# Kernel optimization log

Hardware: AMD Instinct MI355X
Metric: run time of the kernel (lower is better)

## Reference

```python
import jax, jax.numpy as jnp
import numpy as np

D_MODEL = 1024
N_HEAD = 16
D_K = D_MODEL // N_HEAD
NEG = -1e9


def setup_inputs() -> dict:
    key = jax.random.key(0)
    ks = jax.random.split(key, 9)
    B, S = 2, 2048
    scale = 1.0 / np.sqrt(D_MODEL)
    x = jax.random.normal(ks[0], (B, S, D_MODEL), dtype=jnp.float32)
    mask = jnp.tril(jnp.ones((S, S), dtype=jnp.int32))  # causal: 0 => masked
    Wq = jax.random.normal(ks[1], (D_MODEL, D_MODEL), dtype=jnp.float32) * scale
    bq = jnp.zeros((D_MODEL,), dtype=jnp.float32)
    Wk = jax.random.normal(ks[2], (D_MODEL, D_MODEL), dtype=jnp.float32) * scale
    bk = jnp.zeros((D_MODEL,), dtype=jnp.float32)
    Wv = jax.random.normal(ks[3], (D_MODEL, D_MODEL), dtype=jnp.float32) * scale
    bv = jnp.zeros((D_MODEL,), dtype=jnp.float32)
    Wo = jax.random.normal(ks[4], (D_MODEL, D_MODEL), dtype=jnp.float32) * scale
    bo = jnp.zeros((D_MODEL,), dtype=jnp.float32)
    return {"x": x, "mask": mask, "Wq": Wq, "bq": bq, "Wk": Wk, "bk": bk,
            "Wv": Wv, "bv": bv, "Wo": Wo, "bo": bo}


def reference(x, mask, Wq, bq, Wk, bk, Wv, bv, Wo, bo):
    B, S, _ = x.shape
    # torch Linear: y = x @ W.T + b
    def split_heads(y):  # [B,S,D] -> [B,H,S,d_k]
        return y.reshape(B, S, N_HEAD, D_K).transpose(0, 2, 1, 3)
    Q = split_heads(x @ Wq.T + bq)
    K = split_heads(x @ Wk.T + bk)
    V = split_heads(x @ Wv.T + bv)
    scores = jnp.einsum('bhqd,bhkd->bhqk', Q, K) / jnp.sqrt(jnp.float32(D_K))
    scores = jnp.where(mask[None, None, :, :] == 0, jnp.float32(NEG), scores)
    attn = jax.nn.softmax(scores, axis=-1)
    out = jnp.einsum('bhqk,bhkd->bhqd', attn, V)
    out = out.transpose(0, 2, 1, 3).reshape(B, S, D_MODEL)
    return out @ Wo.T + bo
```

## Files before the change

kernel.cpp:

```cpp
#include <hip/hip_runtime.h>
#include <hip/hip_bf16.h>
#include <stdint.h>

#define DM    1024
#define NHEAD 16
#define DKH   64
#define SEQ   2048
#define NB    2
#define MTOT  (NB*SEQ)
#define LSTR  72
#define QSCL  0.18033688f

typedef __hip_bfloat16 bf16;
typedef __attribute__((ext_vector_type(8))) short bf16x8;
typedef __attribute__((ext_vector_type(4))) short bf16x4;
typedef __attribute__((ext_vector_type(4))) float f32x4;
typedef __attribute__((ext_vector_type(4))) uint32_t u32x4;

#define MFMA16(a,b,c) __builtin_amdgcn_mfma_f32_16x16x32_bf16((a),(b),(c),0,0,0)

#if __has_builtin(__builtin_amdgcn_exp2f)
#define EXP2F(x) __builtin_amdgcn_exp2f(x)
#else
#define EXP2F(x) __expf(0.69314718056f * (x))
#endif

__device__ __forceinline__ void async_copy16(const void* g, void* l) {
  __builtin_amdgcn_global_load_lds((const __attribute__((address_space(1))) uint32_t*)g,
                                   (__attribute__((address_space(3))) uint32_t*)l,
                                   16, 0, 0);
}

__device__ __forceinline__ short f32_bf16_bits(float f) {
  uint32_t u = __builtin_bit_cast(uint32_t, f);
  u += 0x7FFFu + ((u >> 16) & 1u);
  return (short)(u >> 16);
}

__device__ __forceinline__ uint32_t pack_bf16x2(float a, float b) {
  return (uint32_t)(uint16_t)f32_bf16_bits(a) |
         ((uint32_t)(uint16_t)f32_bf16_bits(b) << 16);
}

__global__ __launch_bounds__(256) void k_cvt_all(
    const float* __restrict__ x,  const float* __restrict__ Wq,
    const float* __restrict__ Wk, const float* __restrict__ Wv,
    const float* __restrict__ Wo,
    bf16* __restrict__ xb,  bf16* __restrict__ Wqb, bf16* __restrict__ Wkb,
    bf16* __restrict__ Wvb, bf16* __restrict__ Wob) {
  const int NX = (MTOT*DM)/4;
  const int NW = (DM*DM)/4;
  int i = blockIdx.x * 256 + threadIdx.x;
  const float* s; bf16* d; int j; float scl = 1.0f;
  if (i < NX) { s = x; d = xb; j = i; }
  else {
    int t = i - NX;
    int k = t >> 18;
    j = t & (NW - 1);
    s = (k == 0) ? Wq : (k == 1) ? Wk : (k == 2) ? Wv : Wo;
    d = (k == 0) ? Wqb : (k == 1) ? Wkb : (k == 2) ? Wvb : Wob;
    if (k == 0) scl = QSCL;
  }
  float4 v = ((const float4*)s)[j];
  bf16x4 o;
  o[0] = f32_bf16_bits(v.x * scl);
  o[1] = f32_bf16_bits(v.y * scl);
  o[2] = f32_bf16_bits(v.z * scl);
  o[3] = f32_bf16_bits(v.w * scl);
  ((bf16x4*)d)[j] = o;
}

__global__ __launch_bounds__(256) void k_gemm_qkv(
    const bf16* __restrict__ x,
    const bf16* __restrict__ Wq, const bf16* __restrict__ Wk, const bf16* __restrict__ Wv,
    const float* __restrict__ bq, const float* __restrict__ bk, const float* __restrict__ bv,
    bf16* __restrict__ Q, bf16* __restrict__ K, bf16* __restrict__ V) {
  const int id  = blockIdx.x + (blockIdx.y << 5) + (blockIdx.z << 8);
  const int xcd = id & 7;
  const int jj  = id >> 3;
  const int bxi = (xcd << 2) | (jj & 3);
  const int rem = jj >> 2;
  const int byi = rem & 7;
  const int bzi = rem >> 3;

  const bf16* W; const float* bias; bf16* C; float bs;
  if (bzi == 0)      { W = Wq; bias = bq; C = Q; bs = QSCL; }
  else if (bzi == 1) { W = Wk; bias = bk; C = K; bs = 1.0f; }
  else               { W = Wv; bias = bv; C = V; bs = 1.0f; }

  __shared__ __align__(16) short As[128*32];
  __shared__ __align__(16) short Bs[128*32];
  const int tid  = threadIdx.x;
  const int lane = tid & 63;
  const int w    = tid >> 6;
  const int wm   = (w & 1) << 6;
  const int wn   = (w >> 1) << 6;
  const int bm   = bxi << 7;
  const int bn   = byi << 7;
  const int m16  = lane & 15;
  const int quad = lane >> 4;
  const int koff = quad << 3;
  const int c0   = (w << 7) | lane;

  f32x4 acc[4][4] = {};

  for (int k0 = 0; k0 < DM; k0 += 32) {
    __syncthreads();
#pragma unroll
    for (int it = 0; it < 2; ++it) {
      int c   = c0 + (it << 6);
      int row = c >> 2;
      int kc  = c & 3;
      async_copy16(x + (size_t)(bm + row) * DM + k0 + (kc << 3),
                   &As[(size_t)((w << 7) + (it << 6)) << 3]);
      async_copy16(W + (size_t)(bn + row) * DM + k0 + (kc << 3),
                   &Bs[(size_t)((w << 7) + (it << 6)) << 3]);
    }
    __syncthreads();

    bf16x8 af[4], bfv[4];
#pragma unroll
    for (int t = 0; t < 4; ++t)
      af[t]  = *(const bf16x8*)&As[(wm + t*16 + m16) * 32 + koff];
#pragma unroll
    for (int t = 0; t < 4; ++t)
      bfv[t] = *(const bf16x8*)&Bs[(wn + t*16 + m16) * 32 + koff];
#pragma unroll
    for (int i = 0; i < 4; ++i)
#pragma unroll
      for (int j = 0; j < 4; ++j)
        acc[i][j] = MFMA16(af[i], bfv[j], acc[i][j]);
  }

  const int crow0 = bm + wm + (quad << 2);
  const int ccol0 = bn + wn + m16;
#pragma unroll
  for (int j = 0; j < 4; ++j) {
    float bv = bias[ccol0 + j*16] * bs;
#pragma unroll
    for (int i = 0; i < 4; ++i)
#pragma unroll
      for (int r = 0; r < 4; ++r)
        C[(size_t)(crow0 + i*16 + r) * DM + ccol0 + j*16] =
            (bf16)(acc[i][j][r] + bv);
  }
}

__global__ __launch_bounds__(256) void k_gemm_o(
    const bf16* __restrict__ A, const bf16* __restrict__ W,
    const float* __restrict__ bias, float* __restrict__ C) {
  const int id  = blockIdx.x + (blockIdx.y << 5);
  const int xcd = id & 7;
  const int jj  = id >> 3;
  const int bxi = (xcd << 2) | (jj & 3);
  const int byi = jj >> 2;

  __shared__ __align__(16) short As[128*32];
  __shared__ __align__(16) short Bs[64*32];
  const int tid  = threadIdx.x;
  const int lane = tid & 63;
  const int w    = tid >> 6;
  const int wm   = (w & 1) << 6;
  const int wn   = (w >> 1) << 5;
  const int bm   = bxi << 7;
  const int bn   = byi << 6;
  const int m16  = lane & 15;
  const int quad = lane >> 4;
  const int koff = quad << 3;
  const int cA   = (w << 7) | lane;
  const int cB   = (w << 6) | lane;

  f32x4 acc[4][2] = {};

  for (int k0 = 0; k0 < DM; k0 += 32) {
    __syncthreads();
#pragma unroll
    for (int it = 0; it < 2; ++it) {
      int c   = cA + (it << 6);
      int row = c >> 2;
      int kc  = c & 3;
      async_copy16(A + (size_t)(bm + row) * DM + k0 + (kc << 3),
                   &As[(size_t)((w << 7) + (it << 6)) << 3]);
    }
    {
      int row = cB >> 2;
      int kc  = cB & 3;
      async_copy16(W + (size_t)(bn + row) * DM + k0 + (kc << 3),
                   &Bs[(size_t)(w << 6) << 3]);
    }
    __syncthreads();

    bf16x8 af[4], bfv[2];
#pragma unroll
    for (int t = 0; t < 4; ++t)
      af[t]  = *(const bf16x8*)&As[(wm + t*16 + m16) * 32 + koff];
#pragma unroll
    for (int t = 0; t < 2; ++t)
      bfv[t] = *(const bf16x8*)&Bs[(wn + t*16 + m16) * 32 + koff];
#pragma unroll
    for (int i = 0; i < 4; ++i)
#pragma unroll
      for (int j = 0; j < 2; ++j)
        acc[i][j] = MFMA16(af[i], bfv[j], acc[i][j]);
  }

  const int crow0 = bm + wm + (quad << 2);
  const int ccol0 = bn + wn + m16;
#pragma unroll
  for (int j = 0; j < 2; ++j) {
    float bv = bias[ccol0 + j*16];
#pragma unroll
    for (int i = 0; i < 4; ++i)
#pragma unroll
      for (int r = 0; r < 4; ++r)
        C[(size_t)(crow0 + i*16 + r) * DM + ccol0 + j*16] =
            acc[i][j][r] + bv;
  }
}

__global__ __launch_bounds__(256) void k_transpose_v(const bf16* __restrict__ V,
                                                     bf16* __restrict__ Vt) {
  __shared__ __align__(16) short tile[64][LSTR];
  const int tid = threadIdx.x;
  const int s0  = blockIdx.x << 6;
  const int bh  = blockIdx.y;
  const int b   = bh >> 4, h = bh & 15;
#pragma unroll
  for (int it = 0; it < 2; ++it) {
    int c = tid + (it << 8);
    int s = c >> 3, dc = c & 7;
    bf16x8 v = *(const bf16x8*)&V[(size_t)(b*SEQ + s0 + s) * DM + h*DKH + (dc << 3)];
    *(bf16x8*)&tile[s][dc << 3] = v;
  }
  __syncthreads();
#pragma unroll
  for (int it = 0; it < 2; ++it) {
    int c = tid + (it << 8);
    int d = c >> 3, sc = c & 7;
    bf16x8 ov;
#pragma unroll
    for (int i = 0; i < 8; ++i) {
      int p  = (sc << 3) + i;
      int r  = p & 3;
      int st = ((p >> 5) & 1) | (((p >> 2) & 1) << 1);
      int q2 = (p >> 3) & 3;
      ov[i] = tile[st*16 + q2*4 + r][d];
    }
    *(bf16x8*)&Vt[((size_t)bh * DKH + d) * SEQ + s0 + (sc << 3)] = ov;
  }
}

__global__ __launch_bounds__(256) void k_attn(const bf16* __restrict__ Q,
                                              const bf16* __restrict__ K,
                                              const bf16* __restrict__ Vt,
                                              bf16* __restrict__ ctx) {
  __shared__ __align__(16) short Ks[64*LSTR];
  __shared__ __align__(16) short Vs[64*LSTR];

  const int tid  = threadIdx.x;
  const int lane = tid & 63;
  const int w    = tid >> 6;
  const int bh   = blockIdx.y;
  const int mx   = (blockIdx.x ^ bh) & 31;
  const int t64  = (mx & 1) ? (31 - (mx >> 1)) : (mx >> 1);
  const int b    = bh >> 4, h = bh & 15;
  const int m16  = lane & 15, quad = lane >> 4;
  const int koff = quad << 3;

  const int qw    = (t64 << 6) + (w << 4);
  const int ktmax = t64;

  const int r0 = tid >> 3, r1 = r0 + 32, c0 = (tid & 7) << 3;

  const bf16* Kb  = K  + (size_t)(b*SEQ) * DM + h*DKH;
  const bf16* Vtb = Vt + (size_t)bh * DKH * SEQ;

  const bf16* Qb = Q + (size_t)(b*SEQ + qw) * DM + h*DKH;
  bf16x8 qf0 = *(const bf16x8*)(Qb + (size_t)m16*DM + koff);
  bf16x8 qf1 = *(const bf16x8*)(Qb + (size_t)m16*DM + 32 + koff);

  f32x4 o[4] = {};
  float psum = 0.f;
  const int qrow  = qw + m16;
  const int kquad = quad << 2;

  bf16x8 pk0 = *(const bf16x8*)(Kb  + (size_t)r0*DM + c0);
  bf16x8 pk1 = *(const bf16x8*)(Kb  + (size_t)r1*DM + c0);
  bf16x8 pv0 = *(const bf16x8*)(Vtb + (size_t)r0*SEQ + c0);
  bf16x8 pv1 = *(const bf16x8*)(Vtb + (size_t)r1*SEQ + c0);

  for (int kt = 0; kt <= ktmax; ++kt) {
    __syncthreads();
    *(bf16x8*)&Ks[r0*LSTR + c0] = pk0;
    *(bf16x8*)&Ks[r1*LSTR + c0] = pk1;
    *(bf16x8*)&Vs[r0*LSTR + c0] = pv0;
    *(bf16x8*)&Vs[r1*LSTR + c0] = pv1;
    __syncthreads();

    if (kt < ktmax) {
      const int kn = (kt + 1) << 6;
      pk0 = *(const bf16x8*)(Kb  + (size_t)(kn + r0)*DM + c0);
      pk1 = *(const bf16x8*)(Kb  + (size_t)(kn + r1)*DM + c0);
      pv0 = *(const bf16x8*)(Vtb + (size_t)r0*SEQ + kn + c0);
      pv1 = *(const bf16x8*)(Vtb + (size_t)r1*SEQ + kn + c0);
    }

    {
      u32x4 p0, p1;
      const int kbase = (kt << 6) + kquad;
      if (kt == ktmax) {
#pragma unroll
        for (int st = 0; st < 4; ++st) {
          bf16x8 kf0 = *(const bf16x8*)&Ks[(st*16 + m16)*LSTR + koff];
          bf16x8 kf1 = *(const bf16x8*)&Ks[(st*16 + m16)*LSTR + 32 + koff];
          f32x4 a = {};
          a = MFMA16(kf0, qf0, a);
          a = MFMA16(kf1, qf1, a);
          float e[4];
#pragma unroll
          for (int r = 0; r < 4; ++r) {
            float t = EXP2F(a[r]);
            t = (kbase + (st << 4) + r <= qrow) ? t : 0.f;
            e[r] = t; psum += t;
          }
          uint32_t lo = pack_bf16x2(e[0], e[1]);
          uint32_t hi = pack_bf16x2(e[2], e[3]);
          int base = st & 2;
          if (st & 1) { p1[base] = lo; p1[base + 1] = hi; }
          else        { p0[base] = lo; p0[base + 1] = hi; }
        }
      } else {
#pragma unroll
        for (int st = 0; st < 4; ++st) {
          bf16x8 kf0 = *(const bf16x8*)&Ks[(st*16 + m16)*LSTR + koff];
          bf16x8 kf1 = *(const bf16x8*)&Ks[(st*16 + m16)*LSTR + 32 + koff];
          f32x4 a = {};
          a = MFMA16(kf0, qf0, a);
          a = MFMA16(kf1, qf1, a);
          float e[4];
#pragma unroll
          for (int r = 0; r < 4; ++r) {
            float t = EXP2F(a[r]);
            e[r] = t; psum += t;
          }
          uint32_t lo = pack_bf16x2(e[0], e[1]);
          uint32_t hi = pack_bf16x2(e[2], e[3]);
          int base = st & 2;
          if (st & 1) { p1[base] = lo; p1[base + 1] = hi; }
          else        { p0[base] = lo; p0[base + 1] = hi; }
        }
      }
      bf16x8 pa0 = __builtin_bit_cast(bf16x8, p0);
      bf16x8 pa1 = __builtin_bit_cast(bf16x8, p1);
#pragma unroll
      for (int t = 0; t < 4; ++t) {
        bf16x8 vf0 = *(const bf16x8*)&Vs[(t*16 + m16)*LSTR + koff];
        bf16x8 vf1 = *(const bf16x8*)&Vs[(t*16 + m16)*LSTR + 32 + koff];
        o[t] = MFMA16(pa0, vf0, o[t]);
        o[t] = MFMA16(pa1, vf1, o[t]);
      }
    }
  }

  float v = psum;
  v += __shfl_xor(v, 16, 64);
  v += __shfl_xor(v, 32, 64);
  const int lanebase = lane & 48;
  bf16* Cb = ctx + (size_t)(b*SEQ + qw) * DM + h*DKH;
#pragma unroll
  for (int r = 0; r < 4; ++r) {
    float rs  = __shfl(v, lanebase | (kquad | r), 64);
    float inv = 1.0f / rs;
#pragma unroll
    for (int t = 0; t < 4; ++t)
      Cb[(size_t)(kquad + r) * DM + t*16 + m16] = (bf16)(o[t][r] * inv);
  }
}

extern "C" void kernel_launch(void* const* d_in, const int* in_sizes, int n_in,
                              void* d_out, int out_size, void* d_ws, size_t ws_size,
                              hipStream_t stream) {
  const float* x  = (const float*)d_in[0];
  const float* Wq = (const float*)d_in[2];
  const float* bq = (const float*)d_in[3];
  const float* Wk = (const float*)d_in[4];
  const float* bk = (const float*)d_in[5];
  const float* Wv = (const float*)d_in[6];
  const float* bv = (const float*)d_in[7];
  const float* Wo = (const float*)d_in[8];
  const float* bo = (const float*)d_in[9];
  float* out = (float*)d_out;

  const size_t SZ = (size_t)MTOT * DM;
  const size_t WZ = (size_t)DM * DM;
  bf16* xb  = (bf16*)d_ws;
  bf16* Wqb = xb  + SZ;
  bf16* Wkb = Wqb + WZ;
  bf16* Wvb = Wkb + WZ;
  bf16* Wob = Wvb + WZ;
  bf16* Qb  = Wob + WZ;
  bf16* Kb  = Qb  + SZ;
  bf16* Vb  = Kb  + SZ;
  bf16* Vtb = Vb  + SZ;
  bf16* Cx  = xb;

  k_cvt_all<<<(SZ/4 + 4*(WZ/4))/256, 256, 0, stream>>>(
      x, Wq, Wk, Wv, Wo, xb, Wqb, Wkb, Wvb, Wob);

  k_gemm_qkv<<<dim3(MTOT/128, DM/128, 3), 256, 0, stream>>>(
      xb, Wqb, Wkb, Wvb, bq, bk, bv, Qb, Kb, Vb);
  k_transpose_v<<<dim3(SEQ/64, NB*NHEAD), 256, 0, stream>>>(Vb, Vtb);
  k_attn<<<dim3(32, NB*NHEAD), 256, 0, stream>>>(Qb, Kb, Vtb, Cx);
  k_gemm_o<<<dim3(MTOT/128, DM/64), 256, 0, stream>>>(Cx, Wob, bo, out);
}
```

Before: 201.8 us.

## Process two 16-row query tiles per wave in causal attention kernel

Each attention block now covers 128 query rows instead of 64, with each wave computing two 16-row Q tiles against every K/V tile staged in shared memory. This halves K/V loads and LDS reads per query row and raises MFMA work per synchronization. The grid halves to 16 blocks per head, and masking now applies to the last two key tiles. The trade-off is higher register pressure, fewer blocks for occupancy, and coarser causal load balancing.

```diff
diff --git a/kernel.cpp b/kernel.cpp
--- a/kernel.cpp
+++ b/kernel.cpp
@@ -261,14 +261,15 @@
   const int lane = tid & 63;
   const int w    = tid >> 6;
   const int bh   = blockIdx.y;
-  const int mx   = (blockIdx.x ^ bh) & 31;
-  const int t64  = (mx & 1) ? (31 - (mx >> 1)) : (mx >> 1);
+  const int mx   = (blockIdx.x ^ bh) & 15;
+  const int t64  = (mx & 1) ? (15 - (mx >> 1)) : (mx >> 1);
   const int b    = bh >> 4, h = bh & 15;
   const int m16  = lane & 15, quad = lane >> 4;
   const int koff = quad << 3;
 
-  const int qw    = (t64 << 6) + (w << 4);
-  const int ktmax = t64;
+  const int qw    = (t64 << 7) + (w << 5);
+  const int ktmax = 2*t64 + 1;
+  const int kdiag = 2*t64;
 
   const int r0 = tid >> 3, r1 = r0 + 32, c0 = (tid & 7) << 3;
 
@@ -276,12 +277,15 @@
   const bf16* Vtb = Vt + (size_t)bh * DKH * SEQ;
 
   const bf16* Qb = Q + (size_t)(b*SEQ + qw) * DM + h*DKH;
-  bf16x8 qf0 = *(const bf16x8*)(Qb + (size_t)m16*DM + koff);
-  bf16x8 qf1 = *(const bf16x8*)(Qb + (size_t)m16*DM + 32 + koff);
-
-  f32x4 o[4] = {};
-  float psum = 0.f;
-  const int qrow  = qw + m16;
+  bf16x8 qf0a = *(const bf16x8*)(Qb + (size_t)m16*DM + koff);
+  bf16x8 qf1a = *(const bf16x8*)(Qb + (size_t)m16*DM + 32 + koff);
+  bf16x8 qf0b = *(const bf16x8*)(Qb + (size_t)(16 + m16)*DM + koff);
+  bf16x8 qf1b = *(const bf16x8*)(Qb + (size_t)(16 + m16)*DM + 32 + koff);
+
+  f32x4 oa[4] = {}, ob[4] = {};
+  float psa = 0.f, psb = 0.f;
+  const int qrowa = qw + m16;
+  const int qrowb = qw + 16 + m16;
   const int kquad = quad << 2;
 
   bf16x8 pk0 = *(const bf16x8*)(Kb  + (size_t)r0*DM + c0);
@@ -306,74 +310,107 @@
     }
 
     {
-      u32x4 p0, p1;
+      u32x4 p0a, p1a, p0b, p1b;
       const int kbase = (kt << 6) + kquad;
-      if (kt == ktmax) {
+      if (kt >= kdiag) {
 #pragma unroll
         for (int st = 0; st < 4; ++st) {
           bf16x8 kf0 = *(const bf16x8*)&Ks[(st*16 + m16)*LSTR + koff];
           bf16x8 kf1 = *(const bf16x8*)&Ks[(st*16 + m16)*LSTR + 32 + koff];
-          f32x4 a = {};
-          a = MFMA16(kf0, qf0, a);
-          a = MFMA16(kf1, qf1, a);
-          float e[4];
+          f32x4 aa = {}, ab = {};
+          aa = MFMA16(kf0, qf0a, aa);
+          aa = MFMA16(kf1, qf1a, aa);
+          ab = MFMA16(kf0, qf0b, ab);
+          ab = MFMA16(kf1, qf1b, ab);
+          float ea[4], eb[4];
 #pragma unroll
           for (int r = 0; r < 4; ++r) {
-            float t = EXP2F(a[r]);
-            t = (kbase + (st << 4) + r <= qrow) ? t : 0.f;
-            e[r] = t; psum += t;
+            int key = kbase + (st << 4) + r;
+            float ta = EXP2F(aa[r]);
+            ta = (key <= qrowa) ? ta : 0.f;
+            ea[r] = ta; psa += ta;
+            float tb = EXP2F(ab[r]);
+            tb = (key <= qrowb) ? tb : 0.f;
+            eb[r] = tb; psb += tb;
           }
-          uint32_t lo = pack_bf16x2(e[0], e[1]);
-          uint32_t hi = pack_bf16x2(e[2], e[3]);
           int base = st & 2;
-          if (st & 1) { p1[base] = lo; p1[base + 1] = hi; }
-          else        { p0[base] = lo; p0[base + 1] = hi; }
+          uint32_t loa = pack_bf16x2(ea[0], ea[1]);
+          uint32_t hia = pack_bf16x2(ea[2], ea[3]);
+          uint32_t lob = pack_bf16x2(eb[0], eb[1]);
+          uint32_t hib = pack_bf16x2(eb[2], eb[3]);
+          if (st & 1) { p1a[base] = loa; p1a[base+1] = hia;
+                        p1b[base] = lob; p1b[base+1] = hib; }
+          else        { p0a[base] = loa; p0a[base+1] = hia;
+                        p0b[base] = lob; p0b[base+1] = hib; }
         }
       } else {
 #pragma unroll
         for (int st = 0; st < 4; ++st) {
           bf16x8 kf0 = *(const bf16x8*)&Ks[(st*16 + m16)*LSTR + koff];
           bf16x8 kf1 = *(const bf16x8*)&Ks[(st*16 + m16)*LSTR + 32 + koff];
-          f32x4 a = {};
-          a = MFMA16(kf0, qf0, a);
-          a = MFMA16(kf1, qf1, a);
-          float e[4];
+          f32x4 aa = {}, ab = {};
+          aa = MFMA16(kf0, qf0a, aa);
+          aa = MFMA16(kf1, qf1a, aa);
+          ab = MFMA16(kf0, qf0b, ab);
+          ab = MFMA16(kf1, qf1b, ab);
+          float ea[4], eb[4];
 #pragma unroll
           for (int r = 0; r < 4; ++r) {
-            float t = EXP2F(a[r]);
-            e[r] = t; psum += t;
+            float ta = EXP2F(aa[r]);
+            ea[r] = ta; psa += ta;
+            float tb = EXP2F(ab[r]);
+            eb[r] = tb; psb += tb;
           }
-          uint32_t lo = pack_bf16x2(e[0], e[1]);
-          uint32_t hi = pack_bf16x2(e[2], e[3]);
           int base = st & 2;
-          if (st & 1) { p1[base] = lo; p1[base + 1] = hi; }
-          else        { p0[base] = lo; p0[base + 1] = hi; }
+          uint32_t loa = pack_bf16x2(ea[0], ea[1]);
+          uint32_t hia = pack_bf16x2(ea[2], ea[3]);
+          uint32_t lob = pack_bf16x2(eb[0], eb[1]);
+          uint32_t hib = pack_bf16x2(eb[2], eb[3]);
+          if (st & 1) { p1a[base] = loa; p1a[base+1] = hia;
+                        p1b[base] = lob; p1b[base+1] = hib; }
+          else        { p0a[base] = loa; p0a[base+1] = hia;
+                        p0b[base] = lob; p0b[base+1] = hib; }
         }
       }
-      bf16x8 pa0 = __builtin_bit_cast(bf16x8, p0);
-      bf16x8 pa1 = __builtin_bit_cast(bf16x8, p1);
+      bf16x8 pa0a = __builtin_bit_cast(bf16x8, p0a);
+      bf16x8 pa1a = __builtin_bit_cast(bf16x8, p1a);
+      bf16x8 pa0b = __builtin_bit_cast(bf16x8, p0b);
+      bf16x8 pa1b = __builtin_bit_cast(bf16x8, p1b);
 #pragma unroll
       for (int t = 0; t < 4; ++t) {
         bf16x8 vf0 = *(const bf16x8*)&Vs[(t*16 + m16)*LSTR + koff];
         bf16x8 vf1 = *(const bf16x8*)&Vs[(t*16 + m16)*LSTR + 32 + koff];
-        o[t] = MFMA16(pa0, vf0, o[t]);
-        o[t] = MFMA16(pa1, vf1, o[t]);
+        oa[t] = MFMA16(pa0a, vf0, oa[t]);
+        oa[t] = MFMA16(pa1a, vf1, oa[t]);
+        ob[t] = MFMA16(pa0b, vf0, ob[t]);
+        ob[t] = MFMA16(pa1b, vf1, ob[t]);
       }
     }
   }
 
-  float v = psum;
-  v += __shfl_xor(v, 16, 64);
-  v += __shfl_xor(v, 32, 64);
+  float va = psa;
+  va += __shfl_xor(va, 16, 64);
+  va += __shfl_xor(va, 32, 64);
+  float vb = psb;
+  vb += __shfl_xor(vb, 16, 64);
+  vb += __shfl_xor(vb, 32, 64);
   const int lanebase = lane & 48;
   bf16* Cb = ctx + (size_t)(b*SEQ + qw) * DM + h*DKH;
 #pragma unroll
   for (int r = 0; r < 4; ++r) {
-    float rs  = __shfl(v, lanebase | (kquad | r), 64);
-    float inv = 1.0f / rs;
+    float rsa = __shfl(va, lanebase | (kquad | r), 64);
+    float inva = 1.0f / rsa;
 #pragma unroll
     for (int t = 0; t < 4; ++t)
-      Cb[(size_t)(kquad + r) * DM + t*16 + m16] = (bf16)(o[t][r] * inv);
+      Cb[(size_t)(kquad + r) * DM + t*16 + m16] = (bf16)(oa[t][r] * inva);
+  }
+#pragma unroll
+  for (int r = 0; r < 4; ++r) {
+    float rsb = __shfl(vb, lanebase | (kquad | r), 64);
+    float invb = 1.0f / rsb;
+#pragma unroll
+    for (int t = 0; t < 4; ++t)
+      Cb[(size_t)(16 + kquad + r) * DM + t*16 + m16] = (bf16)(ob[t][r] * invb);
   }
 }
 
@@ -410,6 +447,6 @@
   k_gemm_qkv<<<dim3(MTOT/128, DM/128, 3), 256, 0, stream>>>(
       xb, Wqb, Wkb, Wvb, bq, bk, bv, Qb, Kb, Vb);
   k_transpose_v<<<dim3(SEQ/64, NB*NHEAD), 256, 0, stream>>>(Vb, Vtb);
-  k_attn<<<dim3(32, NB*NHEAD), 256, 0, stream>>>(Qb, Kb, Vtb, Cx);
+  k_attn<<<dim3(16, NB*NHEAD), 256, 0, stream>>>(Qb, Kb, Vtb, Cx);
   k_gemm_o<<<dim3(MTOT/128, DM/64), 256, 0, stream>>>(Cx, Wob, bo, out);
 }
```

Measured after the change: 211.0 us. 4.5% more time.

## Process attention key tiles in pairs with doubled LDS staging

Applied to the files above, without the earlier changes.

The attention kernel now stages two 64-key K/V tiles into shared memory per iteration and prefetches the next two tiles into registers, which halves the number of barrier pairs and deepens the global-load prefetch. An odd trailing tile is handled in a separate epilogue with masking. The cost is doubled shared memory per block and more live prefetch registers, which may lower occupancy. Out-of-range prefetches are clamped to the last tile, so some loads are redundant.

```diff
diff --git a/kernel.cpp b/kernel.cpp
--- a/kernel.cpp
+++ b/kernel.cpp
@@ -254,8 +254,10 @@
                                               const bf16* __restrict__ K,
                                               const bf16* __restrict__ Vt,
                                               bf16* __restrict__ ctx) {
-  __shared__ __align__(16) short Ks[64*LSTR];
-  __shared__ __align__(16) short Vs[64*LSTR];
+  __shared__ __align__(16) short KsA[64*LSTR];
+  __shared__ __align__(16) short VsA[64*LSTR];
+  __shared__ __align__(16) short KsB[64*LSTR];
+  __shared__ __align__(16) short VsB[64*LSTR];
 
   const int tid  = threadIdx.x;
   const int lane = tid & 63;
@@ -284,82 +286,116 @@
   const int qrow  = qw + m16;
   const int kquad = quad << 2;
 
-  bf16x8 pk0 = *(const bf16x8*)(Kb  + (size_t)r0*DM + c0);
-  bf16x8 pk1 = *(const bf16x8*)(Kb  + (size_t)r1*DM + c0);
-  bf16x8 pv0 = *(const bf16x8*)(Vtb + (size_t)r0*SEQ + c0);
-  bf16x8 pv1 = *(const bf16x8*)(Vtb + (size_t)r1*SEQ + c0);
-
-  for (int kt = 0; kt <= ktmax; ++kt) {
-    __syncthreads();
-    *(bf16x8*)&Ks[r0*LSTR + c0] = pk0;
-    *(bf16x8*)&Ks[r1*LSTR + c0] = pk1;
-    *(bf16x8*)&Vs[r0*LSTR + c0] = pv0;
-    *(bf16x8*)&Vs[r1*LSTR + c0] = pv1;
-    __syncthreads();
-
-    if (kt < ktmax) {
-      const int kn = (kt + 1) << 6;
-      pk0 = *(const bf16x8*)(Kb  + (size_t)(kn + r0)*DM + c0);
-      pk1 = *(const bf16x8*)(Kb  + (size_t)(kn + r1)*DM + c0);
-      pv0 = *(const bf16x8*)(Vtb + (size_t)r0*SEQ + kn + c0);
-      pv1 = *(const bf16x8*)(Vtb + (size_t)r1*SEQ + kn + c0);
-    }
-
+  auto attn_tile = [&](const short* Kc, const short* Vc, int kt, bool masked) {
+    u32x4 p0, p1;
+    const int kbase = (kt << 6) + kquad;
+    if (masked) {
+#pragma unroll
+      for (int st = 0; st < 4; ++st) {
+        bf16x8 kf0 = *(const bf16x8*)&Kc[(st*16 + m16)*LSTR + koff];
+        bf16x8 kf1 = *(const bf16x8*)&Kc[(st*16 + m16)*LSTR + 32 + koff];
+        f32x4 a = {};
+        a = MFMA16(kf0, qf0, a);
+        a = MFMA16(kf1, qf1, a);
+        float e[4];
+#pragma unroll
+        for (int r = 0; r < 4; ++r) {
+          float t = EXP2F(a[r]);
+          t = (kbase + (st << 4) + r <= qrow) ? t : 0.f;
+          e[r] = t; psum += t;
+        }
+        uint32_t lo = pack_bf16x2(e[0], e[1]);
+        uint32_t hi = pack_bf16x2(e[2], e[3]);
+        int base = st & 2;
+        if (st & 1) { p1[base] = lo; p1[base + 1] = hi; }
+        else        { p0[base] = lo; p0[base + 1] = hi; }
+      }
+    } else {
+#pragma unroll
+      for (int st = 0; st < 4; ++st) {
+        bf16x8 kf0 = *(const bf16x8*)&Kc[(st*16 + m16)*LSTR + koff];
+        bf16x8 kf1 = *(const bf16x8*)&Kc[(st*16 + m16)*LSTR + 32 + koff];
+        f32x4 a = {};
+        a = MFMA16(kf0, qf0, a);
+        a = MFMA16(kf1, qf1, a);
+        float e[4];
+#pragma unroll
+        for (int r = 0; r < 4; ++r) {
+          float t = EXP2F(a[r]);
+          e[r] = t; psum += t;
+        }
+        uint32_t lo = pack_bf16x2(e[0], e[1]);
+        uint32_t hi = pack_bf16x2(e[2], e[3]);
+        int base = st & 2;
+        if (st & 1) { p1[base] = lo; p1[base + 1] = hi; }
+        else        { p0[base] = lo; p0[base + 1] = hi; }
+      }
+    }
+    bf16x8 pa0 = __builtin_bit_cast(bf16x8, p0);
+    bf16x8 pa1 = __builtin_bit_cast(bf16x8, p1);
+#pragma unroll
+    for (int t = 0; t < 4; ++t) {
+      bf16x8 vf0 = *(const bf16x8*)&Vc[(t*16 + m16)*LSTR + koff];
+      bf16x8 vf1 = *(const bf16x8*)&Vc[(t*16 + m16)*LSTR + 32 + koff];
+      o[t] = MFMA16(pa0, vf0, o[t]);
+      o[t] = MFMA16(pa1, vf1, o[t]);
+    }
+  };
+
+  bf16x8 kA0, kA1, vA0, vA1, kB0, kB1, vB0, vB1;
+  {
+    const int kn1 = (ktmax >= 1 ? 1 : 0) << 6;
+    kA0 = *(const bf16x8*)(Kb  + (size_t)r0*DM + c0);
+    kA1 = *(const bf16x8*)(Kb  + (size_t)r1*DM + c0);
+    vA0 = *(const bf16x8*)(Vtb + (size_t)r0*SEQ + c0);
+    vA1 = *(const bf16x8*)(Vtb + (size_t)r1*SEQ + c0);
+    kB0 = *(const bf16x8*)(Kb  + (size_t)(kn1 + r0)*DM + c0);
+    kB1 = *(const bf16x8*)(Kb  + (size_t)(kn1 + r1)*DM + c0);
+    vB0 = *(const bf16x8*)(Vtb + (size_t)r0*SEQ + kn1 + c0);
+    vB1 = *(const bf16x8*)(Vtb + (size_t)r1*SEQ + kn1 + c0);
+  }
+
+  const int ntiles = ktmax + 1;
+  const int npairs = ntiles >> 1;
+
+  for (int p = 0; p < npairs; ++p) {
+    __syncthreads();
+    *(bf16x8*)&KsA[r0*LSTR + c0] = kA0;
+    *(bf16x8*)&KsA[r1*LSTR + c0] = kA1;
+    *(bf16x8*)&VsA[r0*LSTR + c0] = vA0;
+    *(bf16x8*)&VsA[r1*LSTR + c0] = vA1;
+    *(bf16x8*)&KsB[r0*LSTR + c0] = kB0;
+    *(bf16x8*)&KsB[r1*LSTR + c0] = kB1;
+    *(bf16x8*)&VsB[r0*LSTR + c0] = vB0;
+    *(bf16x8*)&VsB[r1*LSTR + c0] = vB1;
+    __syncthreads();
+
+    const int ktA = 2*p, ktB = 2*p + 1;
     {
-      u32x4 p0, p1;
-      const int kbase = (kt << 6) + kquad;
-      if (kt == ktmax) {
-#pragma unroll
-        for (int st = 0; st < 4; ++st) {
-          bf16x8 kf0 = *(const bf16x8*)&Ks[(st*16 + m16)*LSTR + koff];
-          bf16x8 kf1 = *(const bf16x8*)&Ks[(st*16 + m16)*LSTR + 32 + koff];
-          f32x4 a = {};
-          a = MFMA16(kf0, qf0, a);
-          a = MFMA16(kf1, qf1, a);
-          float e[4];
-#pragma unroll
-          for (int r = 0; r < 4; ++r) {
-            float t = EXP2F(a[r]);
-            t = (kbase + (st << 4) + r <= qrow) ? t : 0.f;
-            e[r] = t; psum += t;
-          }
-          uint32_t lo = pack_bf16x2(e[0], e[1]);
-          uint32_t hi = pack_bf16x2(e[2], e[3]);
-          int base = st & 2;
-          if (st & 1) { p1[base] = lo; p1[base + 1] = hi; }
-          else        { p0[base] = lo; p0[base + 1] = hi; }
-        }
-      } else {
-#pragma unroll
-        for (int st = 0; st < 4; ++st) {
-          bf16x8 kf0 = *(const bf16x8*)&Ks[(st*16 + m16)*LSTR + koff];
-          bf16x8 kf1 = *(const bf16x8*)&Ks[(st*16 + m16)*LSTR + 32 + koff];
-          f32x4 a = {};
-          a = MFMA16(kf0, qf0, a);
-          a = MFMA16(kf1, qf1, a);
-          float e[4];
-#pragma unroll
-          for (int r = 0; r < 4; ++r) {
-            float t = EXP2F(a[r]);
-            e[r] = t; psum += t;
-          }
-          uint32_t lo = pack_bf16x2(e[0], e[1]);
-          uint32_t hi = pack_bf16x2(e[2], e[3]);
-          int base = st & 2;
-          if (st & 1) { p1[base] = lo; p1[base + 1] = hi; }
-          else        { p0[base] = lo; p0[base + 1] = hi; }
-        }
-      }
-      bf16x8 pa0 = __builtin_bit_cast(bf16x8, p0);
-      bf16x8 pa1 = __builtin_bit_cast(bf16x8, p1);
-#pragma unroll
-      for (int t = 0; t < 4; ++t) {
-        bf16x8 vf0 = *(const bf16x8*)&Vs[(t*16 + m16)*LSTR + koff];
-        bf16x8 vf1 = *(const bf16x8*)&Vs[(t*16 + m16)*LSTR + 32 + koff];
-        o[t] = MFMA16(pa0, vf0, o[t]);
-        o[t] = MFMA16(pa1, vf1, o[t]);
-      }
-    }
+      const int nA = (ktA + 2 <= ktmax ? ktA + 2 : ktmax) << 6;
+      const int nB = (ktA + 3 <= ktmax ? ktA + 3 : ktmax) << 6;
+      kA0 = *(const bf16x8*)(Kb  + (size_t)(nA + r0)*DM + c0);
+      kA1 = *(const bf16x8*)(Kb  + (size_t)(nA + r1)*DM + c0);
+      vA0 = *(const bf16x8*)(Vtb + (size_t)r0*SEQ + nA + c0);
+      vA1 = *(const bf16x8*)(Vtb + (size_t)r1*SEQ + nA + c0);
+      kB0 = *(const bf16x8*)(Kb  + (size_t)(nB + r0)*DM + c0);
+      kB1 = *(const bf16x8*)(Kb  + (size_t)(nB + r1)*DM + c0);
+      vB0 = *(const bf16x8*)(Vtb + (size_t)r0*SEQ + nB + c0);
+      vB1 = *(const bf16x8*)(Vtb + (size_t)r1*SEQ + nB + c0);
+    }
+
+    attn_tile(KsA, VsA, ktA, false);
+    attn_tile(KsB, VsB, ktB, ktB == ktmax);
+  }
+
+  if (ntiles & 1) {
+    __syncthreads();
+    *(bf16x8*)&KsA[r0*LSTR + c0] = kA0;
+    *(bf16x8*)&KsA[r1*LSTR + c0] = kA1;
+    *(bf16x8*)&VsA[r0*LSTR + c0] = vA0;
+    *(bf16x8*)&VsA[r1*LSTR + c0] = vA1;
+    __syncthreads();
+    attn_tile(KsA, VsA, ktmax, true);
   }
 
   float v = psum;
```

After: 205.7 us. About the same (+1.9%).
